# Kernel optimization log

Measured on AMD Instinct MI355X. Metric: run time of the kernel, lower is better.

The kernel has to match this reference:

```python
import jax, jax.numpy as jnp
import numpy as np

B, IN, H, K = 4096, 1024, 1024, 32  # batch, input_size, hidden_size, inner_hidden


def setup_inputs() -> dict:
    key = jax.random.key(0)
    ks = jax.random.split(key, 11)
    stdv = 1.0 / np.sqrt(H)
    u = lambda k, shp: jax.random.uniform(k, shp, jnp.float32, -stdv, stdv)
    return {
        "x": jax.random.normal(ks[0], (B, IN), jnp.float32),
        "h_prev": jax.random.normal(ks[1], (B, H), jnp.float32),
        "c_prev": jax.random.normal(ks[2], (B, H), jnp.float32),
        "Wg": u(ks[3], (3 * H, IN + H)),
        "bg": u(ks[4], (3 * H,)),
        "Wc": u(ks[5], (2 * H, IN + H)),
        "bc": u(ks[6], (2 * H,)),
        "W1": u(ks[7], (K, 2)),
        "b1": u(ks[8], (K,)),
        "W2": u(ks[9], (1, K)),
        "b2": u(ks[10], (1,)),
    }


def reference(x, h_prev, c_prev, Wg, bg, Wc, bc, W1, b1, W2, b2):
    combined = jnp.concatenate([x, h_prev], axis=1)          # [B, IN+H]
    gates = combined @ Wg.T + bg                              # [B, 3H]
    i, f, o = jnp.split(jax.nn.sigmoid(gates), 3, axis=1)     # each [B, H]
    cell_raw = combined @ Wc.T + bc                           # [B, 2H]
    pairs = cell_raw.reshape(B, H, 2)                         # [B, H, 2]
    hid = jax.nn.relu(jnp.einsum('bhp,kp->bhk', pairs, W1) + b1)  # [B, H, K]
    g = jnp.einsum('bhk,ok->bho', hid, W2)[..., 0] + b2[0]    # [B, H]
    c_next = f * c_prev + i * g
    h_next = o * jnp.tanh(c_next)
    return (h_next, c_next)
```

## Files before the change

### kernel.cpp

```cpp
#include <hip/hip_runtime.h>
#include <hip/hip_bf16.h>

#define BB   4096
#define INW  1024
#define HH   1024
#define KIN  2048
#define NG   5120
#define KH   32
#define FPG  10
#define NTG  32

typedef __bf16 bf16;
typedef __bf16 bf16x4 __attribute__((ext_vector_type(4)));
typedef __bf16 bf16x8 __attribute__((ext_vector_type(8)));
typedef float  floatx4 __attribute__((ext_vector_type(4)));

#define GLD16(gp, lp)                                                          \
  __builtin_amdgcn_global_load_lds(                                            \
      (__attribute__((address_space(1))) const void*)(gp),                     \
      (__attribute__((address_space(3))) void*)(lp), 16, 0, 0)

#define NCB  4096
#define NWB  1280

__global__ __launch_bounds__(256) void prep(
    const float* __restrict__ x, const float* __restrict__ h,
    const float* __restrict__ Wg, const float* __restrict__ Wc,
    bf16* __restrict__ comb, bf16* __restrict__ Wb) {
  int tid = threadIdx.x;
  if (blockIdx.x < NCB) {
    int e = (blockIdx.x * 256 + tid) * 8;
    int b = e >> 11;
    int c = e & (KIN - 1);
    const float* src = (c < INW) ? (x + (size_t)b * INW + c)
                                 : (h + (size_t)b * HH + (c - INW));
    float4 v0 = *(const float4*)src;
    float4 v1 = *(const float4*)(src + 4);
    bf16x8 ov;
    ov[0] = (bf16)v0.x; ov[1] = (bf16)v0.y; ov[2] = (bf16)v0.z; ov[3] = (bf16)v0.w;
    ov[4] = (bf16)v1.x; ov[5] = (bf16)v1.y; ov[6] = (bf16)v1.z; ov[7] = (bf16)v1.w;
    *(bf16x8*)(comb + e) = ov;
  } else {
    int w   = blockIdx.x - NCB;
    int nt  = w / 40;
    int rem = w - nt * 40;
    int f   = rem >> 2;
    int rp  = rem & 3;
    int q   = f / 5;
    int g   = f - q * 5;
    int kk  = tid >> 2;
    int kq  = tid & 3;
    size_t wbase = ((size_t)(nt * FPG + f) * 64 + kk) * 64 + kq * 16;
#pragma unroll
    for (int r4 = 0; r4 < 4; ++r4) {
      int s    = rp * 4 + r4;
      int hcol = nt * 32 + q * 16 + s;
      const float* src = (g < 3)
          ? (Wg + (size_t)(g * HH + hcol) * KIN + tid * 8)
          : (Wc + (size_t)(2 * hcol + (g - 3)) * KIN + tid * 8);
      float4 v0 = *(const float4*)src;
      float4 v1 = *(const float4*)(src + 4);
      bf16x8 ov;
      ov[0] = (bf16)v0.x; ov[1] = (bf16)v0.y; ov[2] = (bf16)v0.z; ov[3] = (bf16)v0.w;
      ov[4] = (bf16)v1.x; ov[5] = (bf16)v1.y; ov[6] = (bf16)v1.z; ov[7] = (bf16)v1.w;
      *(bf16x8*)(Wb + (wbase + s) * 8) = ov;
    }
  }
}

#define ASZ  8192
#define BSZ  10240
#define BUF  (ASZ + BSZ)

__global__ __launch_bounds__(256, 2) void gemm_fused(
    const bf16* __restrict__ A, const bf16* __restrict__ Bm,
    const float* __restrict__ c_prev, const float* __restrict__ bg,
    const float* __restrict__ bc, const float* __restrict__ W1,
    const float* __restrict__ b1, const float* __restrict__ W2,
    const float* __restrict__ b2, float* __restrict__ h_next,
    float* __restrict__ c_next) {
  __shared__ bf16 sh[2 * BUF];

  const int tid  = threadIdx.x;
  const int wave = tid >> 6;
  const int lane = tid & 63;

  const int bid = blockIdx.y * gridDim.x + blockIdx.x;
  const int swz = (bid & 7) * 128 + (bid >> 3);
  const int m0  = (swz & 31) * 128;
  const int nt  = swz >> 5;

  const int wm = (wave >> 1) * 64;
  const int q  = wave & 1;
  const int lr = lane & 15;
  const int qd = lane >> 4;

  floatx4 acc[4][5] = {};

  const int arow0 = tid >> 3;
  const int acol  = (tid & 7);
  const int bf20  = wave;

#define STAGE(bb, kt)                                                          \
  {                                                                            \
    _Pragma("unroll")                                                          \
    for (int j = 0; j < 4; ++j) {                                              \
      int row = arow0 + j * 32;                                                \
      int c   = acol ^ (row & 7);                                              \
      GLD16(A + (size_t)(m0 + row) * KIN + (kt) * 64 + c * 8,                  \
            sh + (size_t)(bb) * BUF + (size_t)(j * 256 + wave * 64) * 8);      \
    }                                                                          \
    _Pragma("unroll")                                                          \
    for (int j = 0; j < 5; ++j) {                                              \
      int c20 = j * 4 + bf20;                                                  \
      int f   = c20 >> 1;                                                      \
      int ks  = c20 & 1;                                                       \
      size_t gchunk = (size_t)(nt * FPG + f) * 64 + ((kt) * 2 + ks);           \
      GLD16(Bm + (gchunk * 64 + lane) * 8,                                     \
            sh + (size_t)(bb) * BUF + ASZ +                                    \
                (size_t)(j * 256 + wave * 64) * 8);                            \
    }                                                                          \
  }

#define COMPUTE(bb)                                                            \
  {                                                                            \
    const bf16* As = sh + (size_t)(bb) * BUF;                                  \
    const bf16* Bs = As + ASZ;                                                 \
    _Pragma("unroll")                                                          \
    for (int ks = 0; ks < 2; ++ks) {                                           \
      bf16x8 af[4];                                                            \
      _Pragma("unroll")                                                        \
      for (int mi = 0; mi < 4; ++mi) {                                         \
        int row  = wm + mi * 16 + lr;                                          \
        int slot = (ks * 4 + qd) ^ (lr & 7);                                   \
        af[mi] = *(const bf16x8*)&As[(row << 6) + (slot << 3)];                \
      }                                                                        \
      bf16x8 bfr[5];                                                           \
      _Pragma("unroll")                                                        \
      for (int ni = 0; ni < 5; ++ni) {                                         \
        int chunk = ((q * 5 + ni) << 1) + ks;                                  \
        bfr[ni] = *(const bf16x8*)&Bs[(chunk << 9) + (lane << 3)];             \
      }                                                                        \
      _Pragma("unroll")                                                        \
      for (int mi = 0; mi < 4; ++mi)                                           \
        _Pragma("unroll")                                                      \
        for (int ni = 0; ni < 5; ++ni)                                         \
          acc[mi][ni] = __builtin_amdgcn_mfma_f32_16x16x32_bf16(               \
              af[mi], bfr[ni], acc[mi][ni], 0, 0, 0);                          \
    }                                                                          \
  }

  STAGE(0, 0);
  __syncthreads();

  for (int kt = 0; kt < KIN / 64 - 1; ++kt) {
    const int cur = kt & 1;
    STAGE(cur ^ 1, kt + 1);
    COMPUTE(cur);
    __syncthreads();
  }
  COMPUTE(1);

  const int h   = nt * 32 + q * 16 + lr;
  const float bgi = bg[h];
  const float bgf = bg[HH + h];
  const float bgo = bg[2 * HH + h];
  const float bc0 = bc[2 * h];
  const float bc1 = bc[2 * h + 1];
  const float gb  = b2[0];

  float p0[16], p1[16], ga[16];
#pragma unroll
  for (int mi = 0; mi < 4; ++mi)
#pragma unroll
    for (int r = 0; r < 4; ++r) {
      p0[mi * 4 + r] = acc[mi][3][r] + bc0;
      p1[mi * 4 + r] = acc[mi][4][r] + bc1;
      ga[mi * 4 + r] = gb;
    }
#pragma unroll
  for (int k = 0; k < KH; ++k) {
    float w0 = W1[2 * k], w1 = W1[2 * k + 1], bk = b1[k], wk = W2[k];
#pragma unroll
    for (int e = 0; e < 16; ++e) {
      float hv = fmaf(p0[e], w0, fmaf(p1[e], w1, bk));
      hv = fmaxf(hv, 0.0f);
      ga[e] = fmaf(hv, wk, ga[e]);
    }
  }

#pragma unroll
  for (int mi = 0; mi < 4; ++mi)
#pragma unroll
    for (int r = 0; r < 4; ++r) {
      int b    = m0 + wm + mi * 16 + qd * 4 + r;
      size_t o = (size_t)b * HH + h;
      float si = 1.0f / (1.0f + __expf(-(acc[mi][0][r] + bgi)));
      float sf = 1.0f / (1.0f + __expf(-(acc[mi][1][r] + bgf)));
      float so = 1.0f / (1.0f + __expf(-(acc[mi][2][r] + bgo)));
      float cn = fmaf(sf, c_prev[o], si * ga[mi * 4 + r]);
      float e2 = __expf(2.0f * cn);
      float th = 1.0f - 2.0f / (e2 + 1.0f);
      h_next[o] = so * th;
      c_next[o] = cn;
    }
}

extern "C" void kernel_launch(void* const* d_in, const int* in_sizes, int n_in,
                              void* d_out, int out_size, void* d_ws, size_t ws_size,
                              hipStream_t stream) {
  const float* x      = (const float*)d_in[0];
  const float* h_prev = (const float*)d_in[1];
  const float* c_prev = (const float*)d_in[2];
  const float* Wg     = (const float*)d_in[3];
  const float* bg     = (const float*)d_in[4];
  const float* Wc     = (const float*)d_in[5];
  const float* bc     = (const float*)d_in[6];
  const float* W1     = (const float*)d_in[7];
  const float* b1     = (const float*)d_in[8];
  const float* W2     = (const float*)d_in[9];
  const float* b2     = (const float*)d_in[10];
  float* out = (float*)d_out;

  char* ws = (char*)d_ws;
  bf16* comb = (bf16*)ws;
  bf16* Wb   = (bf16*)(ws + (size_t)BB * KIN * 2);

  prep<<<NCB + NWB, 256, 0, stream>>>(x, h_prev, Wg, Wc, comb, Wb);

  dim3 grid(BB / 128, NTG);
  gemm_fused<<<grid, 256, 0, stream>>>(comb, Wb, c_prev, bg, bc, W1, b1, W2,
                                       b2, out, out + (size_t)BB * HH);
}
```

Measured before the change: 246.1 us.

## Load B fragments directly into registers instead of staging through LDS

The pre-packed B weight tiles now go straight from global memory into per-wave register double buffers, and only A is staged through shared memory. The K loop is unrolled by two so it can alternate between the register buffers. This cuts LDS traffic and shared-memory footprint for B. In exchange it raises register pressure (20 extra bf16x8 values per thread), which under launch_bounds(256,2) may cause spills, and the two waves sharing each q column set now fetch the same B data from global memory twice instead of once.

Measured after the change: 250.4 us. No clear change (+1.7%).

```diff
diff --git a/kernel.cpp b/kernel.cpp
--- a/kernel.cpp
+++ b/kernel.cpp
@@ -69,8 +69,6 @@
 }
 
 #define ASZ  8192
-#define BSZ  10240
-#define BUF  (ASZ + BSZ)
 
 __global__ __launch_bounds__(256, 2) void gemm_fused(
     const bf16* __restrict__ A, const bf16* __restrict__ Bm,
@@ -79,7 +77,7 @@
     const float* __restrict__ b1, const float* __restrict__ W2,
     const float* __restrict__ b2, float* __restrict__ h_next,
     float* __restrict__ c_next) {
-  __shared__ bf16 sh[2 * BUF];
+  __shared__ bf16 As2[2 * ASZ];
 
   const int tid  = threadIdx.x;
   const int wave = tid >> 6;
@@ -95,37 +93,38 @@
   const int lr = lane & 15;
   const int qd = lane >> 4;
 
+  const bf16* Bq = Bm + (size_t)(nt * FPG + q * 5) * 32768 + (size_t)lane * 8;
+
   floatx4 acc[4][5] = {};
+  bf16x8 bA[2][5], bB[2][5];
 
   const int arow0 = tid >> 3;
-  const int acol  = (tid & 7);
-  const int bf20  = wave;
-
-#define STAGE(bb, kt)                                                          \
+  const int acol  = tid & 7;
+
+#define LOADB(buf, kt)                                                         \
+  {                                                                            \
+    _Pragma("unroll")                                                          \
+    for (int ks = 0; ks < 2; ++ks)                                             \
+      _Pragma("unroll")                                                        \
+      for (int ni = 0; ni < 5; ++ni)                                           \
+        buf[ks][ni] = *(const bf16x8*)(Bq + (size_t)ni * 32768 +               \
+                                       (size_t)((kt) * 2 + ks) * 512);         \
+  }
+
+#define STAGEA(bb, kt)                                                         \
   {                                                                            \
     _Pragma("unroll")                                                          \
     for (int j = 0; j < 4; ++j) {                                              \
       int row = arow0 + j * 32;                                                \
       int c   = acol ^ (row & 7);                                              \
       GLD16(A + (size_t)(m0 + row) * KIN + (kt) * 64 + c * 8,                  \
-            sh + (size_t)(bb) * BUF + (size_t)(j * 256 + wave * 64) * 8);      \
+            As2 + (size_t)(bb) * ASZ + (size_t)(j * 256 + wave * 64) * 8);     \
     }                                                                          \
-    _Pragma("unroll")                                                          \
-    for (int j = 0; j < 5; ++j) {                                              \
-      int c20 = j * 4 + bf20;                                                  \
-      int f   = c20 >> 1;                                                      \
-      int ks  = c20 & 1;                                                       \
-      size_t gchunk = (size_t)(nt * FPG + f) * 64 + ((kt) * 2 + ks);           \
-      GLD16(Bm + (gchunk * 64 + lane) * 8,                                     \
-            sh + (size_t)(bb) * BUF + ASZ +                                    \
-                (size_t)(j * 256 + wave * 64) * 8);                            \
-    }                                                                          \
-  }
-
-#define COMPUTE(bb)                                                            \
+  }
+
+#define COMPUTE(bb, buf)                                                       \
   {                                                                            \
-    const bf16* As = sh + (size_t)(bb) * BUF;                                  \
-    const bf16* Bs = As + ASZ;                                                 \
+    const bf16* As = As2 + (size_t)(bb) * ASZ;                                 \
     _Pragma("unroll")                                                          \
     for (int ks = 0; ks < 2; ++ks) {                                           \
       bf16x8 af[4];                                                            \
@@ -135,31 +134,34 @@
         int slot = (ks * 4 + qd) ^ (lr & 7);                                   \
         af[mi] = *(const bf16x8*)&As[(row << 6) + (slot << 3)];                \
       }                                                                        \
-      bf16x8 bfr[5];                                                           \
-      _Pragma("unroll")                                                        \
-      for (int ni = 0; ni < 5; ++ni) {                                         \
-        int chunk = ((q * 5 + ni) << 1) + ks;                                  \
-        bfr[ni] = *(const bf16x8*)&Bs[(chunk << 9) + (lane << 3)];             \
-      }                                                                        \
       _Pragma("unroll")                                                        \
       for (int mi = 0; mi < 4; ++mi)                                           \
         _Pragma("unroll")                                                      \
         for (int ni = 0; ni < 5; ++ni)                                         \
           acc[mi][ni] = __builtin_amdgcn_mfma_f32_16x16x32_bf16(               \
-              af[mi], bfr[ni], acc[mi][ni], 0, 0, 0);                          \
+              af[mi], buf[ks][ni], acc[mi][ni], 0, 0, 0);                      \
     }                                                                          \
   }
 
-  STAGE(0, 0);
+  LOADB(bA, 0);
+  STAGEA(0, 0);
   __syncthreads();
 
-  for (int kt = 0; kt < KIN / 64 - 1; ++kt) {
-    const int cur = kt & 1;
-    STAGE(cur ^ 1, kt + 1);
-    COMPUTE(cur);
+  for (int kt2 = 0; kt2 < 15; ++kt2) {
+    LOADB(bB, 2 * kt2 + 1);
+    STAGEA(1, 2 * kt2 + 1);
+    COMPUTE(0, bA);
     __syncthreads();
-  }
-  COMPUTE(1);
+    LOADB(bA, 2 * kt2 + 2);
+    STAGEA(0, 2 * kt2 + 2);
+    COMPUTE(1, bB);
+    __syncthreads();
+  }
+  LOADB(bB, 31);
+  STAGEA(1, 31);
+  COMPUTE(0, bA);
+  __syncthreads();
+  COMPUTE(1, bB);
 
   const int h   = nt * 32 + q * 16 + lr;
   const float bgi = bg[h];
```
